# Optimization experiments

Measured on AMD Instinct MI355X. Metric: run time of the kernel, lower is better.

The kernel has to match this reference:

```python
import jax, jax.numpy as jnp
import numpy as np


def setup_inputs() -> dict:
    key = jax.random.key(0)
    x = jax.random.normal(key, (8, 2048, 3), dtype=jnp.float32)
    return {"x": x, "k": 16}


def reference(x, k):
    b, n, d = x.shape
    xf = x.reshape(b * n, d)                      # flatten across batch, as in the torch module
    sq = jnp.sum(xf * xf, axis=1, keepdims=True)  # [BN, 1]
    pair = 2.0 * (xf @ xf.T) - sq - sq.T          # [BN, BN] = -dist^2
    # torch topk(largest=False) on pair == largest of (-pair) == largest squared distance
    neg_vals, idx = jax.lax.top_k(-pair, k + 1)   # [BN, k+1]
    dists = -neg_vals
    dists = dists[:, 1:].reshape(b, n, k)
    idx = idx[:, 1:].reshape(b, n, k)
    return dists, idx
```

## Files before the change

kernel.cpp:

```cpp
#include <hip/hip_runtime.h>
#include <stdint.h>

#define BN       16384
#define NTILES   256
#define NB       64
#define KOUT     16
#define MARGIN   0.01f

typedef float v2f __attribute__((ext_vector_type(2)));
union F4 { float4 f4; v2f p[2]; float f[4]; };

#define WS_TAB    0
#define WS_IDX    (WS_TAB + BN * 16)
#define WS_BND    (WS_IDX + BN * 4)
#define WS_HIST   (WS_BND + NTILES * 8)
#define WS_HMAX   (WS_HIST + 64 * NB * 4)

__device__ __forceinline__ unsigned key_u(unsigned u) {
    return u ^ ((unsigned)((int)u >> 31) | 0x80000000u);
}
__device__ __forceinline__ unsigned wshr1(unsigned v, unsigned oldv) {
    return (unsigned)__builtin_amdgcn_update_dpp((int)oldv, (int)v, 0x138 ,
                                                 0xF, 0xF, false);
}
#define RL16(T) __uint_as_float((unsigned)__builtin_amdgcn_readlane(__float_as_int(T), 16))

__device__ __forceinline__ float sq_of(float gx, float gy, float gz) {
    return __fadd_rn(__fadd_rn(__fmul_rn(gx, gx), __fmul_rn(gy, gy)), __fmul_rn(gz, gz));
}
__device__ __forceinline__ int bucket_of(float sq) {
    const float rho = __fsqrt_rn(sq);
    int b = (int)(64.0f * (1.0f - rho * 0.2f));
    return (b < 0) ? 0 : ((b > 63) ? 63 : b);
}

#define DRAIN(m, p, jvec, T, J)                                                     \
    while (m) {                                                                     \
        const int b_ = (int)__builtin_ctzll(m);                                     \
        m &= m - 1;                                                                 \
        const float pc_ = __uint_as_float(                                          \
            (unsigned)__builtin_amdgcn_readlane(__float_as_int(p), b_));            \
        const unsigned jc_ = (unsigned)__builtin_amdgcn_readlane((int)(jvec), b_);  \
        const float Tup_ =                                                          \
            __uint_as_float(wshr1(__float_as_uint(T), 0xFF800000u ));       \
        const unsigned Jup_ = wshr1((J), 0u);                                       \
        const bool lt_ = (pc_ < Tup_) || ((pc_ == Tup_) && (jc_ < Jup_));           \
        const float Tn_ = lt_ ? Tup_ : pc_;                                         \
        const unsigned Jn_ = lt_ ? Jup_ : jc_;                                      \
        const bool sel_ = (pc_ < (T)) || ((pc_ == (T)) && (jc_ < (J)));             \
        (T) = sel_ ? Tn_ : (T);                                                     \
        (J) = sel_ ? Jn_ : (J);                                                     \
    }

#define EVALC(c, d2)                                                                \
    asm("v_pk_mul_f32 %0, %1, %2 op_sel:[0,0] op_sel_hi:[0,1]"                      \
        : "=v"(d2) : "v"((c).p[0]), "v"(c0A));                                      \
    asm("v_pk_fma_f32 %0, %1, %2, %0 op_sel:[1,0,0] op_sel_hi:[1,1,1]"              \
        : "+v"(d2) : "v"((c).p[0]), "v"(c1A));                                      \
    asm("v_pk_fma_f32 %0, %1, %2, %0 op_sel:[0,0,0] op_sel_hi:[0,1,1]"              \
        : "+v"(d2) : "v"((c).p[1]), "v"(c2A));                                      \
    asm("v_pk_add_f32 %0, %0, %1" : "+v"(d2) : "v"(nsq01));                         \
    asm("v_pk_add_f32 %0, %0, %1 op_sel:[0,1] op_sel_hi:[1,1]"                      \
        : "+v"(d2) : "v"((c).p[1]));

#define CERTM(bd)                                                                    \
    __ballot((__builtin_fmaf(twor0, (bd)[1], __fadd_rn(sq0, (bd)[0])) < thr0) &&     \
             (__builtin_fmaf(twor1, (bd)[1], __fadd_rn(sq1, (bd)[0])) < thr1))

#define COMPUTE_TSTAR()                                                              \
    do {                                                                             \
        uint64_t mm;                                                                 \
        if ((mm = CERTM(bdA)))        ts = (int)__builtin_ctzll(mm);                 \
        else if ((mm = CERTM(bdB)))   ts = 64  + (int)__builtin_ctzll(mm);           \
        else if ((mm = CERTM(bdC)))   ts = 128 + (int)__builtin_ctzll(mm);           \
        else if ((mm = CERTM(bdD)))   ts = 192 + (int)__builtin_ctzll(mm);           \
        else                          ts = NTILES;                                   \
    } while (0)

#define PROC1(c, t)                                                                  \
    {                                                                                \
        v2f d2; EVALC(c, d2)                                                         \
        uint64_t m0 = __ballot(d2[0] <= fF0);                                        \
        uint64_t m1 = __ballot(d2[1] <= fF1);                                        \
        if (m0 | m1) {                                                               \
            const unsigned jvec = (unsigned)idx16[(t) * 64 + lane];                  \
            const float p0v = d2[0], p1v = d2[1];                                    \
            DRAIN(m0, p0v, jvec, T0, J0)                                             \
            DRAIN(m1, p1v, jvec, T1, J1)                                             \
            fF0 = RL16(T0); thr0 = __fsub_rn(-fF0, MARGIN);                          \
            fF1 = RL16(T1); thr1 = __fsub_rn(-fF1, MARGIN);                          \
            COMPUTE_TSTAR();                                                         \
        }                                                                            \
    }

__device__ __forceinline__ void presort64(float p, unsigned j, int lane, double* sw,
                                          float& T, unsigned& J) {
    const double dm = (double)key_u(__float_as_uint(p)) * 16384.0 + (double)j;
    sw[lane] = dm;
    unsigned rank = 0;
    const char* sb = (const char*)sw;
    unsigned off = (unsigned)lane * 8u;
#pragma unroll 7
    for (int s = 1; s < 64; ++s) {
        off = (off + 8u) & 511u;
        const double dn = *(const double*)(sb + off);
        rank += (dn < dm) ? 1u : 0u;
    }
    sw[rank] = __longlong_as_double(
        (long long)(((unsigned long long)j << 32) | __float_as_uint(p)));
    const unsigned long long v = (unsigned long long)__double_as_longlong(sw[lane]);
    T = __uint_as_float((unsigned)(v & 0xFFFFFFFFull));
    J = (unsigned)(v >> 32);
}

__global__ __launch_bounds__(256) void k_hist(const float* __restrict__ x,
                                              unsigned* __restrict__ hist,
                                              unsigned* __restrict__ hmax) {
    __shared__ unsigned h[NB], m[NB];
    const int tid = threadIdx.x;
    if (tid < NB) { h[tid] = 0u; m[tid] = 0u; }
    __syncthreads();
    const int i = blockIdx.x * 256 + tid;
    const float sq = sq_of(x[3 * i], x[3 * i + 1], x[3 * i + 2]);
    const int b = bucket_of(sq);
    atomicAdd(&h[b], 1u);
    atomicMax(&m[b], __float_as_uint(sq));
    __syncthreads();
    if (tid < NB) {
        hist[blockIdx.x * NB + tid] = h[tid];
        hmax[blockIdx.x * NB + tid] = m[tid];
    }
}

__global__ __launch_bounds__(256) void k_prep(const float* __restrict__ x,
                                              const unsigned* __restrict__ hist,
                                              const unsigned* __restrict__ hmax,
                                              float4* __restrict__ tab,
                                              unsigned short* __restrict__ idx16,
                                              float2* __restrict__ bnd) {
    __shared__ unsigned colbase[NB], cur[NB], basev[NB + 1], mxv[NB], sfxs[NB];
    const int tid = threadIdx.x;
    const int blk = blockIdx.x;
    if (tid < NB) {
        unsigned tot = 0u, part = 0u, mx = 0u;
#pragma unroll 8
        for (int g = 0; g < 64; ++g) {
            const unsigned h = hist[g * NB + tid];
            tot += h;
            part += (g < blk) ? h : 0u;
            const unsigned w = hmax[g * NB + tid];
            mx = (w > mx) ? w : mx;
        }
        unsigned v = tot;
#pragma unroll
        for (int s = 1; s < 64; s <<= 1) {
            const unsigned n = (unsigned)__shfl_up((int)v, (unsigned)s, 64);
            v += (tid >= s) ? n : 0u;
        }
        basev[tid] = v - tot;
        if (tid == NB - 1) basev[NB] = v;
        colbase[tid] = (v - tot) + part;
        cur[tid] = 0u;
        mxv[tid] = mx;
    }
    __syncthreads();
    const int i = blk * 256 + tid;
    const float gx = x[3 * i], gy = x[3 * i + 1], gz = x[3 * i + 2];
    const float sq = sq_of(gx, gy, gz);
    const int b = bucket_of(sq);
    const unsigned r = atomicAdd(&cur[b], 1u);
    const unsigned pos = colbase[b] + r;
    tab[pos] = make_float4(gx, gy, gz, -sq);
    idx16[pos] = (unsigned short)i;

    if (blk == 0) {
        if (tid == 0) {
            unsigned M = 0u;
            for (int b2 = NB - 1; b2 >= 0; --b2) {
                const unsigned w = mxv[b2];
                M = (w > M) ? w : M;
                sfxs[b2] = M;
            }
        }
        __syncthreads();
        const unsigned posb = (unsigned)tid * 64u;
        int bb = 0;
        for (int t2 = 0; t2 < NB; ++t2)
            if (basev[t2] <= posb && posb < basev[t2 + 1]) bb = t2;
        const float B = __uint_as_float(sfxs[bb]);
        const float sqB_up = __uint_as_float(__float_as_uint(__fsqrt_rn(B)) + 2u);
        bnd[tid] = make_float2(B, sqB_up);
    }
}

__global__ __launch_bounds__(256) void knn_far_kernel(
    const float4* __restrict__ tab, const unsigned short* __restrict__ idx16,
    const float2* __restrict__ bnd, float* __restrict__ out_d, float* __restrict__ out_i) {
    __shared__ double swall[4 * 64];
    const int tid  = threadIdx.x;
    const int lane = tid & 63;
    const int wid  = tid >> 6;
    double* sw = swall + wid * 64;
    const int p0 = (blockIdx.x * 4 + wid) * 2;
    const int p1 = p0 + 1;

    F4 qa; qa.f4 = tab[p0];
    F4 qb; qb.f4 = tab[p1];
    const unsigned q0 = (unsigned)idx16[p0];
    const unsigned q1 = (unsigned)idx16[p1];
    const float sq0 = -qa.f[3], sq1 = -qb.f[3];
    const v2f nsq01 = {qa.f[3], qb.f[3]};
    const v2f c0A = {2.0f * qa.f[0], 2.0f * qb.f[0]};
    const v2f c1A = {2.0f * qa.f[1], 2.0f * qb.f[1]};
    const v2f c2A = {2.0f * qa.f[2], 2.0f * qb.f[2]};
    const float twor0 = 2.0f * __uint_as_float(__float_as_uint(__fsqrt_rn(sq0)) + 2u);
    const float twor1 = 2.0f * __uint_as_float(__float_as_uint(__fsqrt_rn(sq1)) + 2u);

    const v2f* bndv = (const v2f*)bnd;
    const v2f bdA = bndv[lane];
    const v2f bdB = bndv[64 + lane];
    const v2f bdC = bndv[128 + lane];
    const v2f bdD = bndv[192 + lane];

    float T0, T1; unsigned J0, J1;
    float fF0, fF1, thr0, thr1;
    int ts = NTILES;

    {
        F4 s0_, s1_, s2_, s3_;
        s0_.f4 = tab[0 * 64 + lane];
        s1_.f4 = tab[1 * 64 + lane];
        s2_.f4 = tab[2 * 64 + lane];
        s3_.f4 = tab[3 * 64 + lane];
        const unsigned jv0 = (unsigned)idx16[lane];
        {
            v2f d2; EVALC(s0_, d2)
            presort64(d2[0], jv0, lane, sw, T0, J0);
            presort64(d2[1], jv0, lane, sw, T1, J1);
            fF0 = RL16(T0); thr0 = __fsub_rn(-fF0, MARGIN);
            fF1 = RL16(T1); thr1 = __fsub_rn(-fF1, MARGIN);
        }
        PROC1(s1_, 1)
        PROC1(s2_, 2)
        PROC1(s3_, 3)
    }

    COMPUTE_TSTAR();

    for (int t = 4; t < ts; t += 4) {
        F4 cA_, cB_, cC_, cD_;
        cA_.f4 = tab[(t + 0) * 64 + lane];
        cB_.f4 = tab[(t + 1) * 64 + lane];
        cC_.f4 = tab[(t + 2) * 64 + lane];
        cD_.f4 = tab[(t + 3) * 64 + lane];
        PROC1(cA_, t + 0)
        PROC1(cB_, t + 1)
        PROC1(cC_, t + 2)
        PROC1(cD_, t + 3)
    }

    if (lane >= 1 && lane <= KOUT) {
        const int r = lane - 1;
        out_d[q0 * KOUT + r] = T0;
        out_i[q0 * KOUT + r] = (float)J0;
        out_d[q1 * KOUT + r] = T1;
        out_i[q1 * KOUT + r] = (float)J1;
    }
}

extern "C" void kernel_launch(void* const* d_in, const int* in_sizes, int n_in,
                              void* d_out, int out_size, void* d_ws, size_t ws_size,
                              hipStream_t stream) {
    const float* x = (const float*)d_in[0];
    char* ws = (char*)d_ws;
    float4*         tab   = (float4*)(ws + WS_TAB);
    unsigned short* idx16 = (unsigned short*)(ws + WS_IDX);
    float2*         bnd   = (float2*)(ws + WS_BND);
    unsigned*       hist  = (unsigned*)(ws + WS_HIST);
    unsigned*       hmax  = (unsigned*)(ws + WS_HMAX);
    float* out_d = (float*)d_out;
    float* out_i = out_d + (size_t)BN * KOUT;

    hipLaunchKernelGGL(k_hist, dim3(64), dim3(256), 0, stream, x, hist, hmax);
    hipLaunchKernelGGL(k_prep, dim3(64), dim3(256), 0, stream, x, hist, hmax,
                       tab, idx16, bnd);
    hipLaunchKernelGGL(knn_far_kernel, dim3(BN / 8), dim3(256), 0, stream,
                       tab, idx16, bnd, out_d, out_i);
}
```

Measured before the change: 77.32 us.

## Merge histogram and bucket-scatter prep into a single one-block kernel

```diff
diff --git a/kernel.cpp b/kernel.cpp
--- a/kernel.cpp
+++ b/kernel.cpp
@@ -13,8 +13,6 @@
 #define WS_TAB    0
 #define WS_IDX    (WS_TAB + BN * 16)
 #define WS_BND    (WS_IDX + BN * 4)
-#define WS_HIST   (WS_BND + NTILES * 8)
-#define WS_HMAX   (WS_HIST + 64 * NB * 4)
 
 __device__ __forceinline__ unsigned key_u(unsigned u) {
     return u ^ ((unsigned)((int)u >> 31) | 0x80000000u);
@@ -113,44 +111,34 @@
     J = (unsigned)(v >> 32);
 }
 
-__global__ __launch_bounds__(256) void k_hist(const float* __restrict__ x,
-                                              unsigned* __restrict__ hist,
-                                              unsigned* __restrict__ hmax) {
-    __shared__ unsigned h[NB], m[NB];
+__global__ __launch_bounds__(256) void k_prep1(const float* __restrict__ x,
+                                               float4* __restrict__ tab,
+                                               unsigned short* __restrict__ idx16,
+                                               float2* __restrict__ bnd) {
+    __shared__ unsigned hc[4][NB];
+    __shared__ unsigned hm[NB];
+    __shared__ unsigned basev[NB + 1], cursor[NB], sfxs[NB];
     const int tid = threadIdx.x;
-    if (tid < NB) { h[tid] = 0u; m[tid] = 0u; }
+    const int wid = tid >> 6;
+    if (tid < NB) {
+        hc[0][tid] = 0u; hc[1][tid] = 0u; hc[2][tid] = 0u; hc[3][tid] = 0u;
+        hm[tid] = 0u;
+    }
     __syncthreads();
-    const int i = blockIdx.x * 256 + tid;
-    const float sq = sq_of(x[3 * i], x[3 * i + 1], x[3 * i + 2]);
-    const int b = bucket_of(sq);
-    atomicAdd(&h[b], 1u);
-    atomicMax(&m[b], __float_as_uint(sq));
+
+#pragma unroll 4
+    for (int j = 0; j < 64; ++j) {
+        const int i = j * 256 + tid;
+        const float gx = x[3 * i], gy = x[3 * i + 1], gz = x[3 * i + 2];
+        const float sq = sq_of(gx, gy, gz);
+        const int b = bucket_of(sq);
+        atomicAdd(&hc[wid][b], 1u);
+        atomicMax(&hm[b], __float_as_uint(sq));
+    }
     __syncthreads();
+
     if (tid < NB) {
-        hist[blockIdx.x * NB + tid] = h[tid];
-        hmax[blockIdx.x * NB + tid] = m[tid];
-    }
-}
-
-__global__ __launch_bounds__(256) void k_prep(const float* __restrict__ x,
-                                              const unsigned* __restrict__ hist,
-                                              const unsigned* __restrict__ hmax,
-                                              float4* __restrict__ tab,
-                                              unsigned short* __restrict__ idx16,
-                                              float2* __restrict__ bnd) {
-    __shared__ unsigned colbase[NB], cur[NB], basev[NB + 1], mxv[NB], sfxs[NB];
-    const int tid = threadIdx.x;
-    const int blk = blockIdx.x;
-    if (tid < NB) {
-        unsigned tot = 0u, part = 0u, mx = 0u;
-#pragma unroll 8
-        for (int g = 0; g < 64; ++g) {
-            const unsigned h = hist[g * NB + tid];
-            tot += h;
-            part += (g < blk) ? h : 0u;
-            const unsigned w = hmax[g * NB + tid];
-            mx = (w > mx) ? w : mx;
-        }
+        const unsigned tot = hc[0][tid] + hc[1][tid] + hc[2][tid] + hc[3][tid];
         unsigned v = tot;
 #pragma unroll
         for (int s = 1; s < 64; s <<= 1) {
@@ -158,31 +146,31 @@
             v += (tid >= s) ? n : 0u;
         }
         basev[tid] = v - tot;
+        cursor[tid] = v - tot;
         if (tid == NB - 1) basev[NB] = v;
-        colbase[tid] = (v - tot) + part;
-        cur[tid] = 0u;
-        mxv[tid] = mx;
+    }
+    if (tid == 0) {
+        unsigned M = 0u;
+        for (int b2 = NB - 1; b2 >= 0; --b2) {
+            const unsigned w = hm[b2];
+            M = (w > M) ? w : M;
+            sfxs[b2] = M;
+        }
     }
     __syncthreads();
-    const int i = blk * 256 + tid;
-    const float gx = x[3 * i], gy = x[3 * i + 1], gz = x[3 * i + 2];
-    const float sq = sq_of(gx, gy, gz);
-    const int b = bucket_of(sq);
-    const unsigned r = atomicAdd(&cur[b], 1u);
-    const unsigned pos = colbase[b] + r;
-    tab[pos] = make_float4(gx, gy, gz, -sq);
-    idx16[pos] = (unsigned short)i;
-
-    if (blk == 0) {
-        if (tid == 0) {
-            unsigned M = 0u;
-            for (int b2 = NB - 1; b2 >= 0; --b2) {
-                const unsigned w = mxv[b2];
-                M = (w > M) ? w : M;
-                sfxs[b2] = M;
-            }
-        }
-        __syncthreads();
+
+#pragma unroll 4
+    for (int j = 0; j < 64; ++j) {
+        const int i = j * 256 + tid;
+        const float gx = x[3 * i], gy = x[3 * i + 1], gz = x[3 * i + 2];
+        const float sq = sq_of(gx, gy, gz);
+        const int b = bucket_of(sq);
+        const unsigned pos = atomicAdd(&cursor[b], 1u);
+        tab[pos] = make_float4(gx, gy, gz, -sq);
+        idx16[pos] = (unsigned short)i;
+    }
+
+    {
         const unsigned posb = (unsigned)tid * 64u;
         int bb = 0;
         for (int t2 = 0; t2 < NB; ++t2)
@@ -276,14 +264,10 @@
     float4*         tab   = (float4*)(ws + WS_TAB);
     unsigned short* idx16 = (unsigned short*)(ws + WS_IDX);
     float2*         bnd   = (float2*)(ws + WS_BND);
-    unsigned*       hist  = (unsigned*)(ws + WS_HIST);
-    unsigned*       hmax  = (unsigned*)(ws + WS_HMAX);
     float* out_d = (float*)d_out;
     float* out_i = out_d + (size_t)BN * KOUT;
 
-    hipLaunchKernelGGL(k_hist, dim3(64), dim3(256), 0, stream, x, hist, hmax);
-    hipLaunchKernelGGL(k_prep, dim3(64), dim3(256), 0, stream, x, hist, hmax,
-                       tab, idx16, bnd);
+    hipLaunchKernelGGL(k_prep1, dim3(1), dim3(256), 0, stream, x, tab, idx16, bnd);
     hipLaunchKernelGGL(knn_far_kernel, dim3(BN / 8), dim3(256), 0, stream,
                        tab, idx16, bnd, out_d, out_i);
 }
```

Result: slower. 105.3 us (+36.2%).
